# Kernel tuning notes

Hardware: AMD Instinct MI355X
Metric: run time of the kernel (lower is better)

Reference implementation:

```python
import itertools
import jax, jax.numpy as jnp
import numpy as np

NUM_LEVELS = 16
LEVEL_DIM = 2
LOG2_HASH = 19
BASE_RES = 16          # torch-ngp default base_resolution
DESIRED_RES = 513      # Grid passes desired_resolution + 1 to the encoder
GRID_RES = 512         # Grid.self.resolution


def _levels():
    # replicates torch-ngp GridEncoder offset construction (align_corners=False)
    scale = np.exp2(np.log2(DESIRED_RES / BASE_RES) / (NUM_LEVELS - 1))
    max_params = 2 ** LOG2_HASH
    levels, offset = [], 0
    for i in range(NUM_LEVELS):
        res = int(np.ceil(BASE_RES * scale ** i))
        n = min(max_params, (res + 1) ** 3)
        n = int(np.ceil(n / 8) * 8)  # round up to multiple of 8
        levels.append((res, n, offset))
        offset += n
    return levels, offset

LEVELS, TOTAL_PARAMS = _levels()  # TOTAL_PARAMS == 5295344
CORNERS = np.array(list(itertools.product([0, 1], repeat=3)), dtype=np.int32)  # [8,3]


def hashgrid_encode(x, table):
    """torch-ngp multires hash grid, linear interpolation, align_corners=False.
    x: [M,3] in [0,1]; table: [TOTAL_PARAMS, LEVEL_DIM]. Returns [M, 32]."""
    feats = []
    for (R, H, O) in LEVELS:
        pos = x * R + 0.5                       # [M,3]
        pg = jnp.floor(pos).astype(jnp.int32)   # grid cell (no grad)
        frac = pos - pg.astype(pos.dtype)       # [M,3] trilinear fracs
        lvl = jnp.zeros((x.shape[0], LEVEL_DIM), x.dtype)
        linear = (R + 1) ** 3 <= H              # tight grid vs hashed level
        for c in CORNERS:
            corner = pg + jnp.asarray(c)        # [M,3]
            if linear:
                idx = (corner[:, 0]
                       + corner[:, 1] * (R + 1)
                       + corner[:, 2] * (R + 1) ** 2) % H
            else:
                cu = corner.astype(jnp.uint32)
                # instant-NGP fast_hash primes {1, 2654435761, 805459861}
                idx = ((cu[:, 0] * jnp.uint32(1))
                       ^ (cu[:, 1] * jnp.uint32(2654435761))
                       ^ (cu[:, 2] * jnp.uint32(805459861))) % jnp.uint32(H)
                idx = idx.astype(jnp.int32)
            w = jnp.prod(jnp.where(jnp.asarray(c)[None, :] == 1, frac, 1.0 - frac), axis=-1)
            lvl = lvl + w[:, None] * table[O + idx]
        feats.append(lvl)
    return jnp.concatenate(feats, axis=-1)      # [M, 16*2]


def setup_inputs() -> dict:
    key = jax.random.key(0)
    k1, k2, k3, k4 = jax.random.split(key, 4)
    N = 262144
    bound = jnp.ones((1,), jnp.float32)
    xyz = (jax.random.uniform(k1, (N, 3), jnp.float32) * 2.0 - 1.0) * bound
    table = jax.random.normal(k2, (TOTAL_PARAMS, LEVEL_DIM), jnp.float32) * 0.1
    w1 = jax.random.normal(k3, (NUM_LEVELS * LEVEL_DIM, 64), jnp.float32) * (2.0 / (NUM_LEVELS * LEVEL_DIM)) ** 0.5
    w2 = jax.random.normal(k4, (64, 8), jnp.float32) * (2.0 / 64) ** 0.5
    return {"xyz": xyz, "bound": bound, "table": table, "w1": w1, "w2": w2}


def reference(xyz, bound, table, w1, w2):
    N = xyz.shape[0]
    x = (xyz + bound) / (2.0 * bound)           # normalize to [0,1]
    coords = x * GRID_RES
    c0 = jnp.clip(jnp.floor(coords), 0, GRID_RES - 1).astype(jnp.int32)  # [N,3]
    uvw = coords - c0.astype(coords.dtype)      # (u,v,w) outer trilinear fracs
    offs = jnp.asarray(CORNERS)                 # [8,3]
    corners = c0[None, :, :] + offs[:, None, :]                 # [8,N,3] int grid pts
    enc_in = corners.astype(jnp.float32) / GRID_RES             # [8,N,3] in [0,1]
    feats = hashgrid_encode(enc_in.reshape(-1, 3), table)       # [8N,32]
    f = jax.nn.relu(feats @ w1) @ w2                            # tiny bias-free MLP
    f = f.reshape(8, N, -1)                                     # [8,N,8]
    # corner (ax,ay,az) weight = prod_d (uvw_d if a_d else 1-uvw_d)
    wts = jnp.prod(jnp.where(offs[:, None, :] == 1, uvw[None], 1.0 - uvw[None]), axis=-1)  # [8,N]
    return jnp.sum(wts[..., None] * f, axis=0)                  # [N,8]
```

## Files before the change

### kernel.cpp

```cpp
#include <hip/hip_runtime.h>
#include <stdint.h>


#define BLK 256

#define R15 513

__constant__ int   c_hO[9] = {576752, 1101040, 1625328, 2149616, 2673904,
                              3198192, 3722480, 4246768, 4771056};
__constant__ float c_hR[9] = {81.f, 102.f, 129.f, 162.f, 204.f, 257.f,
                              324.f, 408.f, (float)R15};

template <int R, int H, int O>
__device__ __forceinline__ void enc_linear(float xcx, float xcy, float xcz,
                                           const float2* __restrict__ tab,
                                           float& f0, float& f1) {
    const float Rf = (float)R;
    float px = __fadd_rn(__fmul_rn(xcx, Rf), 0.5f);
    float py = __fadd_rn(__fmul_rn(xcy, Rf), 0.5f);
    float pz = __fadd_rn(__fmul_rn(xcz, Rf), 0.5f);
    float fpx = floorf(px), fpy = floorf(py), fpz = floorf(pz);
    float frx = px - fpx, fry = py - fpy, frz = pz - fpz;
    int gx = (int)fpx, gy = (int)fpy, gz = (int)fpz;
    float wx[2] = {1.f - frx, frx};
    float wy[2] = {1.f - fry, fry};
    float wz[2] = {1.f - frz, frz};
    float a0 = 0.f, a1 = 0.f;
#pragma unroll
    for (int c = 0; c < 8; ++c) {
        const int ox = (c >> 2) & 1, oy = (c >> 1) & 1, oz = c & 1;
        int id  = (gx + ox) + (gy + oy) * (R + 1) + (gz + oz) * ((R + 1) * (R + 1));
        int idx = id % H;
        float w = wx[ox] * wy[oy] * wz[oz];
        float2 tv = tab[O + idx];
        a0 = fmaf(w, tv.x, a0);
        a1 = fmaf(w, tv.y, a1);
    }
    f0 = a0; f1 = a1;
}

__global__ __launch_bounds__(BLK, 4)
void grid_fused(const float* __restrict__ xyz, const float* __restrict__ bound,
                const float* __restrict__ table, const float* __restrict__ w1,
                const float* __restrict__ w2, float* __restrict__ out, int N) {
    __shared__ float sfeat[32 * BLK];

    const int tid = threadIdx.x;
    const int t = blockIdx.x * BLK + tid;
    const int p = t >> 3;
    const int a = t & 7;
    if (p >= N) return;

    const float2* tab = (const float2*)table;

    const float b = bound[0];
    float X = xyz[3 * p + 0], Y = xyz[3 * p + 1], Z = xyz[3 * p + 2];
    float cx = ((X + b) / (2.0f * b)) * 512.0f;
    float cy = ((Y + b) / (2.0f * b)) * 512.0f;
    float cz = ((Z + b) / (2.0f * b)) * 512.0f;
    float c0x = fmaxf(fminf(floorf(cx), 511.f), 0.f);
    float c0y = fmaxf(fminf(floorf(cy), 511.f), 0.f);
    float c0z = fmaxf(fminf(floorf(cz), 511.f), 0.f);
    float uu = cx - c0x, vv = cy - c0y, wwf = cz - c0z;

    const int ax = (a >> 2) & 1, ay = (a >> 1) & 1, az = a & 1;
    float xcx = (c0x + (float)ax) * (1.0f / 512.0f);
    float xcy = (c0y + (float)ay) * (1.0f / 512.0f);
    float xcz = (c0z + (float)az) * (1.0f / 512.0f);

    float f0, f1;
    enc_linear<16,   4920,      0>(xcx, xcy, xcz, tab, f0, f1); sfeat[ 0*BLK+tid]=f0; sfeat[ 1*BLK+tid]=f1;
    enc_linear<21,  10648,   4920>(xcx, xcy, xcz, tab, f0, f1); sfeat[ 2*BLK+tid]=f0; sfeat[ 3*BLK+tid]=f1;
    enc_linear<26,  19688,  15568>(xcx, xcy, xcz, tab, f0, f1); sfeat[ 4*BLK+tid]=f0; sfeat[ 5*BLK+tid]=f1;
    enc_linear<33,  39304,  35256>(xcx, xcy, xcz, tab, f0, f1); sfeat[ 6*BLK+tid]=f0; sfeat[ 7*BLK+tid]=f1;
    enc_linear<41,  74088,  74560>(xcx, xcy, xcz, tab, f0, f1); sfeat[ 8*BLK+tid]=f0; sfeat[ 9*BLK+tid]=f1;
    enc_linear<51, 140608, 148648>(xcx, xcy, xcz, tab, f0, f1); sfeat[10*BLK+tid]=f0; sfeat[11*BLK+tid]=f1;
    enc_linear<65, 287496, 289256>(xcx, xcy, xcz, tab, f0, f1); sfeat[12*BLK+tid]=f0; sfeat[13*BLK+tid]=f1;

#pragma unroll 1
    for (int l = 0; l < 9; ++l) {
        const float Rf = c_hR[l];
        const int   O  = c_hO[l];
        float px = __fadd_rn(__fmul_rn(xcx, Rf), 0.5f);
        float py = __fadd_rn(__fmul_rn(xcy, Rf), 0.5f);
        float pz = __fadd_rn(__fmul_rn(xcz, Rf), 0.5f);
        float fpx = floorf(px), fpy = floorf(py), fpz = floorf(pz);
        float frx = px - fpx, fry = py - fpy, frz = pz - fpz;
        uint32_t gx = (uint32_t)(int)fpx, gy = (uint32_t)(int)fpy, gz = (uint32_t)(int)fpz;
        float wx[2] = {1.f - frx, frx};
        float wy[2] = {1.f - fry, fry};
        float wz[2] = {1.f - frz, frz};
        float a0 = 0.f, a1 = 0.f;
#pragma unroll
        for (int c = 0; c < 8; ++c) {
            const int ox = (c >> 2) & 1, oy = (c >> 1) & 1, oz = c & 1;
            uint32_t idx = ((gx + (uint32_t)ox) ^
                            ((gy + (uint32_t)oy) * 2654435761u) ^
                            ((gz + (uint32_t)oz) * 805459861u)) & 524287u;
            float w = wx[ox] * wy[oy] * wz[oz];
            float2 tv = tab[O + (int)idx];
            a0 = fmaf(w, tv.x, a0);
            a1 = fmaf(w, tv.y, a1);
        }
        sfeat[(14 + 2 * l) * BLK + tid] = a0;
        sfeat[(15 + 2 * l) * BLK + tid] = a1;
    }

    float acc[8] = {0.f, 0.f, 0.f, 0.f, 0.f, 0.f, 0.f, 0.f};
#pragma unroll 1
    for (int kb = 0; kb < 64; kb += 32) {
        float h[32];
#pragma unroll
        for (int k = 0; k < 32; ++k) h[k] = 0.f;
#pragma unroll 1
        for (int i = 0; i < 32; ++i) {
            float fi = sfeat[i * BLK + tid];
            const float* wr = w1 + i * 64 + kb;
#pragma unroll
            for (int k = 0; k < 32; ++k) h[k] = fmaf(fi, wr[k], h[k]);
        }
#pragma unroll
        for (int k = 0; k < 32; ++k) {
            float hk = fmaxf(h[k], 0.f);
            const float* w2r = w2 + (kb + k) * 8;
#pragma unroll
            for (int j = 0; j < 8; ++j) acc[j] = fmaf(hk, w2r[j], acc[j]);
        }
    }

    float wt = (ax ? uu : 1.f - uu) * (ay ? vv : 1.f - vv) * (az ? wwf : 1.f - wwf);
#pragma unroll
    for (int j = 0; j < 8; ++j) {
        float v = acc[j] * wt;
        v += __shfl_xor(v, 1);
        v += __shfl_xor(v, 2);
        v += __shfl_xor(v, 4);
        acc[j] = v;
    }
    float r01 = (a & 1) ? acc[1] : acc[0];
    float r23 = (a & 1) ? acc[3] : acc[2];
    float r45 = (a & 1) ? acc[5] : acc[4];
    float r67 = (a & 1) ? acc[7] : acc[6];
    float r03 = (a & 2) ? r23 : r01;
    float r47 = (a & 2) ? r67 : r45;
    float r   = (a & 4) ? r47 : r03;
    out[t] = r;
}

extern "C" void kernel_launch(void* const* d_in, const int* in_sizes, int n_in,
                              void* d_out, int out_size, void* d_ws, size_t ws_size,
                              hipStream_t stream) {
    const float* xyz   = (const float*)d_in[0];
    const float* bound = (const float*)d_in[1];
    const float* table = (const float*)d_in[2];
    const float* w1    = (const float*)d_in[3];
    const float* w2    = (const float*)d_in[4];
    float* out = (float*)d_out;

    const int N = in_sizes[0] / 3;
    const int threads = N * 8;
    const int blocks = (threads + BLK - 1) / BLK;
    grid_fused<<<blocks, BLK, 0, stream>>>(xyz, bound, table, w1, w2, out, N);
}
```

Before: 395.8 us.

## Run first MLP layer on MFMA with split-fp16 precision and per-wave LDS staging

Moves the 32x64 first MLP layer from scalar FMAs onto 16x16x32 fp16 MFMA instructions. Features and weights are split into hi/lo fp16 pairs and combined over three MFMAs to approximate fp32 accuracy. Features are staged in a per-wave LDS layout, and hidden activations are written back to LDS for the ReLU and second-layer FMAs. Hash levels are fully unrolled with constexpr tables, row hash products are precomputed, and the bounds check is removed, so N*8 must be a multiple of the block size. Occupancy launch bounds are lowered from 4 to 3 blocks.

```diff
diff --git a/kernel.cpp b/kernel.cpp
--- a/kernel.cpp
+++ b/kernel.cpp
@@ -3,162 +3,221 @@
 
 
 #define BLK 256
-
 #define R15 513
-
-__constant__ int   c_hO[9] = {576752, 1101040, 1625328, 2149616, 2673904,
-                              3198192, 3722480, 4246768, 4771056};
-__constant__ float c_hR[9] = {81.f, 102.f, 129.f, 162.f, 204.f, 257.f,
-                              324.f, 408.f, (float)R15};
+#define WSTRIDE 9216
+
+typedef _Float16 half8  __attribute__((ext_vector_type(8)));
+typedef _Float16 half2v __attribute__((ext_vector_type(2)));
+typedef float    floatx4 __attribute__((ext_vector_type(4)));
+
+__device__ __forceinline__ void split16(float x, _Float16& hi, _Float16& lo) {
+  hi = (_Float16)x;
+  lo = (_Float16)(x - (float)hi);
+}
+
+__device__ __forceinline__ void store_feat(char* wb, int lane, int l,
+                                           float a0, float a1) {
+  _Float16 h0, l0, h1, l1;
+  split16(a0, h0, l0);
+  split16(a1, h1, l1);
+  int lin = ((lane >> 4) * 4 + (l >> 2)) * 16 + (lane & 15);
+  int off = lin * 16 + (l & 3) * 4;
+  *(half2v*)(wb + off)        = (half2v){h0, h1};
+  *(half2v*)(wb + 4096 + off) = (half2v){l0, l1};
+}
 
 template <int R, int H, int O>
 __device__ __forceinline__ void enc_linear(float xcx, float xcy, float xcz,
                                            const float2* __restrict__ tab,
-                                           float& f0, float& f1) {
-    const float Rf = (float)R;
+                                           float& o0, float& o1) {
+  const float Rf = (float)R;
+  float px = __fadd_rn(__fmul_rn(xcx, Rf), 0.5f);
+  float py = __fadd_rn(__fmul_rn(xcy, Rf), 0.5f);
+  float pz = __fadd_rn(__fmul_rn(xcz, Rf), 0.5f);
+  float fpx = floorf(px), fpy = floorf(py), fpz = floorf(pz);
+  float frx = px - fpx, fry = py - fpy, frz = pz - fpz;
+  int gx = (int)fpx, gy = (int)fpy, gz = (int)fpz;
+  int ty0 = gy * (R + 1), ty1 = ty0 + (R + 1);
+  int tz0 = gz * ((R + 1) * (R + 1)), tz1 = tz0 + (R + 1) * (R + 1);
+  float wx[2] = {1.f - frx, frx};
+  float wy[2] = {1.f - fry, fry};
+  float wz[2] = {1.f - frz, frz};
+  float a0 = 0.f, a1 = 0.f;
+#pragma unroll
+  for (int c = 0; c < 8; ++c) {
+    const int ox = (c >> 2) & 1, oy = (c >> 1) & 1, oz = c & 1;
+    int id  = (gx + ox) + (oy ? ty1 : ty0) + (oz ? tz1 : tz0);
+    int idx = id % H;
+    float w = wx[ox] * wy[oy] * wz[oz];
+    float2 tv = tab[O + idx];
+    a0 = fmaf(w, tv.x, a0);
+    a1 = fmaf(w, tv.y, a1);
+  }
+  o0 = a0; o1 = a1;
+}
+
+__global__ __launch_bounds__(BLK, 3)
+void grid_fused(const float* __restrict__ xyz, const float* __restrict__ bound,
+                const float* __restrict__ table, const float* __restrict__ w1,
+                const float* __restrict__ w2, float* __restrict__ out) {
+  __shared__ __align__(16) char smem[36864];
+
+  const int tid  = threadIdx.x;
+  const int lane = tid & 63;
+  const int wv   = tid >> 6;
+  const int t    = blockIdx.x * BLK + tid;
+  const int p    = t >> 3;
+  const int a    = t & 7;
+
+  const float2* tab = (const float2*)table;
+  char* wb = smem + wv * WSTRIDE;
+
+  const float b = bound[0];
+  float X = xyz[3 * p + 0], Y = xyz[3 * p + 1], Z = xyz[3 * p + 2];
+  float cx = ((X + b) / (2.0f * b)) * 512.0f;
+  float cy = ((Y + b) / (2.0f * b)) * 512.0f;
+  float cz = ((Z + b) / (2.0f * b)) * 512.0f;
+  float c0x = fmaxf(fminf(floorf(cx), 511.f), 0.f);
+  float c0y = fmaxf(fminf(floorf(cy), 511.f), 0.f);
+  float c0z = fmaxf(fminf(floorf(cz), 511.f), 0.f);
+  float uu = cx - c0x, vv = cy - c0y, wwf = cz - c0z;
+
+  const int ax = (a >> 2) & 1, ay = (a >> 1) & 1, az = a & 1;
+  float xcx = (c0x + (float)ax) * (1.0f / 512.0f);
+  float xcy = (c0y + (float)ay) * (1.0f / 512.0f);
+  float xcz = (c0z + (float)az) * (1.0f / 512.0f);
+
+  {
+    float f0, f1;
+    enc_linear<16,   4920,      0>(xcx, xcy, xcz, tab, f0, f1); store_feat(wb, lane, 0, f0, f1);
+    enc_linear<21,  10648,   4920>(xcx, xcy, xcz, tab, f0, f1); store_feat(wb, lane, 1, f0, f1);
+    enc_linear<26,  19688,  15568>(xcx, xcy, xcz, tab, f0, f1); store_feat(wb, lane, 2, f0, f1);
+    enc_linear<33,  39304,  35256>(xcx, xcy, xcz, tab, f0, f1); store_feat(wb, lane, 3, f0, f1);
+    enc_linear<41,  74088,  74560>(xcx, xcy, xcz, tab, f0, f1); store_feat(wb, lane, 4, f0, f1);
+    enc_linear<51, 140608, 148648>(xcx, xcy, xcz, tab, f0, f1); store_feat(wb, lane, 5, f0, f1);
+    enc_linear<65, 287496, 289256>(xcx, xcy, xcz, tab, f0, f1); store_feat(wb, lane, 6, f0, f1);
+  }
+
+  constexpr int   hO[9] = {576752, 1101040, 1625328, 2149616, 2673904,
+                           3198192, 3722480, 4246768, 4771056};
+  constexpr float hR[9] = {81.f, 102.f, 129.f, 162.f, 204.f, 257.f,
+                           324.f, 408.f, (float)R15};
+#pragma unroll
+  for (int l = 0; l < 9; ++l) {
+    const float Rf = hR[l];
+    const int   O  = hO[l];
     float px = __fadd_rn(__fmul_rn(xcx, Rf), 0.5f);
     float py = __fadd_rn(__fmul_rn(xcy, Rf), 0.5f);
     float pz = __fadd_rn(__fmul_rn(xcz, Rf), 0.5f);
     float fpx = floorf(px), fpy = floorf(py), fpz = floorf(pz);
     float frx = px - fpx, fry = py - fpy, frz = pz - fpz;
-    int gx = (int)fpx, gy = (int)fpy, gz = (int)fpz;
+    uint32_t gx = (uint32_t)(int)fpx, gy = (uint32_t)(int)fpy, gz = (uint32_t)(int)fpz;
+    uint32_t hy0 = gy * 2654435761u, hy1 = (gy + 1u) * 2654435761u;
+    uint32_t hz0 = gz * 805459861u,  hz1 = (gz + 1u) * 805459861u;
     float wx[2] = {1.f - frx, frx};
     float wy[2] = {1.f - fry, fry};
     float wz[2] = {1.f - frz, frz};
     float a0 = 0.f, a1 = 0.f;
 #pragma unroll
     for (int c = 0; c < 8; ++c) {
-        const int ox = (c >> 2) & 1, oy = (c >> 1) & 1, oz = c & 1;
-        int id  = (gx + ox) + (gy + oy) * (R + 1) + (gz + oz) * ((R + 1) * (R + 1));
-        int idx = id % H;
-        float w = wx[ox] * wy[oy] * wz[oz];
-        float2 tv = tab[O + idx];
-        a0 = fmaf(w, tv.x, a0);
-        a1 = fmaf(w, tv.y, a1);
-    }
-    f0 = a0; f1 = a1;
-}
-
-__global__ __launch_bounds__(BLK, 4)
-void grid_fused(const float* __restrict__ xyz, const float* __restrict__ bound,
-                const float* __restrict__ table, const float* __restrict__ w1,
-                const float* __restrict__ w2, float* __restrict__ out, int N) {
-    __shared__ float sfeat[32 * BLK];
-
-    const int tid = threadIdx.x;
-    const int t = blockIdx.x * BLK + tid;
-    const int p = t >> 3;
-    const int a = t & 7;
-    if (p >= N) return;
-
-    const float2* tab = (const float2*)table;
-
-    const float b = bound[0];
-    float X = xyz[3 * p + 0], Y = xyz[3 * p + 1], Z = xyz[3 * p + 2];
-    float cx = ((X + b) / (2.0f * b)) * 512.0f;
-    float cy = ((Y + b) / (2.0f * b)) * 512.0f;
-    float cz = ((Z + b) / (2.0f * b)) * 512.0f;
-    float c0x = fmaxf(fminf(floorf(cx), 511.f), 0.f);
-    float c0y = fmaxf(fminf(floorf(cy), 511.f), 0.f);
-    float c0z = fmaxf(fminf(floorf(cz), 511.f), 0.f);
-    float uu = cx - c0x, vv = cy - c0y, wwf = cz - c0z;
-
-    const int ax = (a >> 2) & 1, ay = (a >> 1) & 1, az = a & 1;
-    float xcx = (c0x + (float)ax) * (1.0f / 512.0f);
-    float xcy = (c0y + (float)ay) * (1.0f / 512.0f);
-    float xcz = (c0z + (float)az) * (1.0f / 512.0f);
-
-    float f0, f1;
-    enc_linear<16,   4920,      0>(xcx, xcy, xcz, tab, f0, f1); sfeat[ 0*BLK+tid]=f0; sfeat[ 1*BLK+tid]=f1;
-    enc_linear<21,  10648,   4920>(xcx, xcy, xcz, tab, f0, f1); sfeat[ 2*BLK+tid]=f0; sfeat[ 3*BLK+tid]=f1;
-    enc_linear<26,  19688,  15568>(xcx, xcy, xcz, tab, f0, f1); sfeat[ 4*BLK+tid]=f0; sfeat[ 5*BLK+tid]=f1;
-    enc_linear<33,  39304,  35256>(xcx, xcy, xcz, tab, f0, f1); sfeat[ 6*BLK+tid]=f0; sfeat[ 7*BLK+tid]=f1;
-    enc_linear<41,  74088,  74560>(xcx, xcy, xcz, tab, f0, f1); sfeat[ 8*BLK+tid]=f0; sfeat[ 9*BLK+tid]=f1;
-    enc_linear<51, 140608, 148648>(xcx, xcy, xcz, tab, f0, f1); sfeat[10*BLK+tid]=f0; sfeat[11*BLK+tid]=f1;
-    enc_linear<65, 287496, 289256>(xcx, xcy, xcz, tab, f0, f1); sfeat[12*BLK+tid]=f0; sfeat[13*BLK+tid]=f1;
-
-#pragma unroll 1
-    for (int l = 0; l < 9; ++l) {
-        const float Rf = c_hR[l];
-        const int   O  = c_hO[l];
-        float px = __fadd_rn(__fmul_rn(xcx, Rf), 0.5f);
-        float py = __fadd_rn(__fmul_rn(xcy, Rf), 0.5f);
-        float pz = __fadd_rn(__fmul_rn(xcz, Rf), 0.5f);
-        float fpx = floorf(px), fpy = floorf(py), fpz = floorf(pz);
-        float frx = px - fpx, fry = py - fpy, frz = pz - fpz;
-        uint32_t gx = (uint32_t)(int)fpx, gy = (uint32_t)(int)fpy, gz = (uint32_t)(int)fpz;
-        float wx[2] = {1.f - frx, frx};
-        float wy[2] = {1.f - fry, fry};
-        float wz[2] = {1.f - frz, frz};
-        float a0 = 0.f, a1 = 0.f;
-#pragma unroll
-        for (int c = 0; c < 8; ++c) {
-            const int ox = (c >> 2) & 1, oy = (c >> 1) & 1, oz = c & 1;
-            uint32_t idx = ((gx + (uint32_t)ox) ^
-                            ((gy + (uint32_t)oy) * 2654435761u) ^
-                            ((gz + (uint32_t)oz) * 805459861u)) & 524287u;
-            float w = wx[ox] * wy[oy] * wz[oz];
-            float2 tv = tab[O + (int)idx];
-            a0 = fmaf(w, tv.x, a0);
-            a1 = fmaf(w, tv.y, a1);
-        }
-        sfeat[(14 + 2 * l) * BLK + tid] = a0;
-        sfeat[(15 + 2 * l) * BLK + tid] = a1;
-    }
-
-    float acc[8] = {0.f, 0.f, 0.f, 0.f, 0.f, 0.f, 0.f, 0.f};
-#pragma unroll 1
-    for (int kb = 0; kb < 64; kb += 32) {
-        float h[32];
-#pragma unroll
-        for (int k = 0; k < 32; ++k) h[k] = 0.f;
-#pragma unroll 1
-        for (int i = 0; i < 32; ++i) {
-            float fi = sfeat[i * BLK + tid];
-            const float* wr = w1 + i * 64 + kb;
-#pragma unroll
-            for (int k = 0; k < 32; ++k) h[k] = fmaf(fi, wr[k], h[k]);
-        }
-#pragma unroll
-        for (int k = 0; k < 32; ++k) {
-            float hk = fmaxf(h[k], 0.f);
-            const float* w2r = w2 + (kb + k) * 8;
-#pragma unroll
-            for (int j = 0; j < 8; ++j) acc[j] = fmaf(hk, w2r[j], acc[j]);
-        }
-    }
-
-    float wt = (ax ? uu : 1.f - uu) * (ay ? vv : 1.f - vv) * (az ? wwf : 1.f - wwf);
+      const int ox = (c >> 2) & 1, oy = (c >> 1) & 1, oz = c & 1;
+      uint32_t idx = ((gx + (uint32_t)ox) ^ (oy ? hy1 : hy0) ^ (oz ? hz1 : hz0))
+                     & 524287u;
+      float w = wx[ox] * wy[oy] * wz[oz];
+      float2 tv = tab[O + (int)idx];
+      a0 = fmaf(w, tv.x, a0);
+      a1 = fmaf(w, tv.y, a1);
+    }
+    store_feat(wb, lane, 7 + l, a0, a1);
+  }
+
+  const int col  = lane & 15;
+  const int quad = lane >> 4;
+
+  half8 ahi[4], alo[4];
+#pragma unroll
+  for (int r = 0; r < 4; ++r) {
+    int off = ((r * 4 + quad) * 16 + col) * 16;
+    ahi[r] = *(const half8*)(wb + off);
+    alo[r] = *(const half8*)(wb + 4096 + off);
+  }
+  __builtin_amdgcn_wave_barrier();
+
+  half8 b1hi[4], b1lo[4];
+#pragma unroll
+  for (int nt = 0; nt < 4; ++nt)
 #pragma unroll
     for (int j = 0; j < 8; ++j) {
-        float v = acc[j] * wt;
-        v += __shfl_xor(v, 1);
-        v += __shfl_xor(v, 2);
-        v += __shfl_xor(v, 4);
-        acc[j] = v;
-    }
-    float r01 = (a & 1) ? acc[1] : acc[0];
-    float r23 = (a & 1) ? acc[3] : acc[2];
-    float r45 = (a & 1) ? acc[5] : acc[4];
-    float r67 = (a & 1) ? acc[7] : acc[6];
-    float r03 = (a & 2) ? r23 : r01;
-    float r47 = (a & 2) ? r67 : r45;
-    float r   = (a & 4) ? r47 : r03;
-    out[t] = r;
+      _Float16 hi, lo;
+      split16(w1[(quad * 8 + j) * 64 + nt * 16 + col], hi, lo);
+      b1hi[nt][j] = hi; b1lo[nt][j] = lo;
+    }
+
+  float* hbuf = (float*)wb;
+  float acc[8] = {0.f, 0.f, 0.f, 0.f, 0.f, 0.f, 0.f, 0.f};
+
+#pragma unroll
+  for (int hf = 0; hf < 2; ++hf) {
+#pragma unroll
+    for (int r = 0; r < 4; ++r) {
+#pragma unroll
+      for (int tt = 0; tt < 2; ++tt) {
+        const int nt = 2 * hf + tt;
+        floatx4 d = __builtin_amdgcn_mfma_f32_16x16x32_f16(
+            ahi[r], b1hi[nt], (floatx4){0.f, 0.f, 0.f, 0.f}, 0, 0, 0);
+        d = __builtin_amdgcn_mfma_f32_16x16x32_f16(ahi[r], b1lo[nt], d, 0, 0, 0);
+        d = __builtin_amdgcn_mfma_f32_16x16x32_f16(alo[r], b1hi[nt], d, 0, 0, 0);
+#pragma unroll
+        for (int i = 0; i < 4; ++i)
+          hbuf[(r * 16 + quad * 4 + i) * 36 + tt * 16 + col] = d[i];
+      }
+    }
+    __builtin_amdgcn_wave_barrier();
+    const char* hrow = wb + lane * 144;
+#pragma unroll
+    for (int c4 = 0; c4 < 8; ++c4) {
+      floatx4 hv = *(const floatx4*)(hrow + c4 * 16);
+#pragma unroll
+      for (int e = 0; e < 4; ++e) {
+        float hk = fmaxf(hv[e], 0.f);
+        const float* w2r = w2 + (hf * 32 + c4 * 4 + e) * 8;
+#pragma unroll
+        for (int j = 0; j < 8; ++j) acc[j] = fmaf(hk, w2r[j], acc[j]);
+      }
+    }
+    __builtin_amdgcn_wave_barrier();
+  }
+
+  float wt = (ax ? uu : 1.f - uu) * (ay ? vv : 1.f - vv) * (az ? wwf : 1.f - wwf);
+#pragma unroll
+  for (int j = 0; j < 8; ++j) {
+    float v = acc[j] * wt;
+    v += __shfl_xor(v, 1);
+    v += __shfl_xor(v, 2);
+    v += __shfl_xor(v, 4);
+    acc[j] = v;
+  }
+  float r01 = (a & 1) ? acc[1] : acc[0];
+  float r23 = (a & 1) ? acc[3] : acc[2];
+  float r45 = (a & 1) ? acc[5] : acc[4];
+  float r67 = (a & 1) ? acc[7] : acc[6];
+  float r03 = (a & 2) ? r23 : r01;
+  float r47 = (a & 2) ? r67 : r45;
+  float r   = (a & 4) ? r47 : r03;
+  out[t] = r;
 }
 
 extern "C" void kernel_launch(void* const* d_in, const int* in_sizes, int n_in,
                               void* d_out, int out_size, void* d_ws, size_t ws_size,
                               hipStream_t stream) {
-    const float* xyz   = (const float*)d_in[0];
-    const float* bound = (const float*)d_in[1];
-    const float* table = (const float*)d_in[2];
-    const float* w1    = (const float*)d_in[3];
-    const float* w2    = (const float*)d_in[4];
-    float* out = (float*)d_out;
-
-    const int N = in_sizes[0] / 3;
-    const int threads = N * 8;
-    const int blocks = (threads + BLK - 1) / BLK;
-    grid_fused<<<blocks, BLK, 0, stream>>>(xyz, bound, table, w1, w2, out, N);
-}
+  const float* xyz   = (const float*)d_in[0];
+  const float* bound = (const float*)d_in[1];
+  const float* table = (const float*)d_in[2];
+  const float* w1    = (const float*)d_in[3];
+  const float* w2    = (const float*)d_in[4];
+  float* out = (float*)d_out;
+
+  const int N = in_sizes[0] / 3;
+  const int blocks = (N * 8) / BLK;
+  grid_fused<<<blocks, BLK, 0, stream>>>(xyz, bound, table, w1, w2, out);
+}
```

Measured after the change: 398.9 us. No clear change (+0.8%).
